# Kernel optimization log

Measured on AMD Instinct MI355X. Metric: run time of the kernel, lower is better.

Reference implementation:

```python
import jax, jax.numpy as jnp
import numpy as np

B, T, H = 256, 2048, 128
LSTM_IN = [24, 128, 128]


def _xavier(key, fan_out, fan_in):
    std = (2.0 / (fan_in + fan_out)) ** 0.5
    return jax.random.normal(key, (fan_out, fan_in), jnp.float32) * std


def setup_inputs() -> dict:
    key = jax.random.key(0)
    ks = jax.random.split(key, 32)
    inp = {}
    inp['scent'] = jax.random.normal(ks[0], (B, T, 3), jnp.float32)
    # fc1: Linear(3,12) + ReLU + Linear(12,24) + ReLU, xavier weights, zero bias
    inp['W1'] = _xavier(ks[1], 12, 3); inp['b1'] = jnp.zeros((12,), jnp.float32)
    inp['W2'] = _xavier(ks[2], 24, 12); inp['b2'] = jnp.zeros((24,), jnp.float32)
    # 3-layer LSTM, PyTorch default init: uniform(-1/sqrt(H), 1/sqrt(H)) for all params
    k = 1.0 / np.sqrt(H)
    for l in range(3):
        d = LSTM_IN[l]
        inp[f'Wih{l}'] = jax.random.uniform(ks[4 + 4 * l], (4 * H, d), jnp.float32, -k, k)
        inp[f'Whh{l}'] = jax.random.uniform(ks[5 + 4 * l], (4 * H, H), jnp.float32, -k, k)
        inp[f'bih{l}'] = jax.random.uniform(ks[6 + 4 * l], (4 * H,), jnp.float32, -k, k)
        inp[f'bhh{l}'] = jax.random.uniform(ks[7 + 4 * l], (4 * H,), jnp.float32, -k, k)
    # fc2: Linear(128,64) + ReLU + Linear(64,32) + ReLU
    inp['Wf1'] = _xavier(ks[20], 64, 128); inp['bf1'] = jnp.zeros((64,), jnp.float32)
    inp['Wf2'] = _xavier(ks[21], 32, 64); inp['bf2'] = jnp.zeros((32,), jnp.float32)
    return inp


def _lstm_layer(x, Wih, Whh, bih, bhh):
    # x: [T, B, D] -> ys: [T, B, H]; PyTorch gate order i, f, g, o
    gx = jnp.einsum('tbd,gd->tbg', x, Wih) + bih + bhh  # [T, B, 4H]

    def step(carry, g_t):
        h, c = carry
        gates = g_t + h @ Whh.T
        i, f, g, o = jnp.split(gates, 4, axis=-1)
        c = jax.nn.sigmoid(f) * c + jax.nn.sigmoid(i) * jnp.tanh(g)
        h = jax.nn.sigmoid(o) * jnp.tanh(c)
        return (h, c), h

    h0 = jnp.zeros((x.shape[1], H), x.dtype)
    (hT, cT), ys = jax.lax.scan(step, (h0, h0), gx)
    return ys, hT, cT


def reference(scent, W1, b1, W2, b2,
              Wih0, Whh0, bih0, bhh0,
              Wih1, Whh1, bih1, bhh1,
              Wih2, Whh2, bih2, bhh2,
              Wf1, bf1, Wf2, bf2):
    # fc1 (pointwise over B*T)
    x = jax.nn.relu(scent @ W1.T + b1)
    x = jax.nn.relu(x @ W2.T + b2)          # [B, T, 24]
    x = jnp.transpose(x, (1, 0, 2))          # [T, B, 24] seq-first
    hs, cs = [], []
    for Wih, Whh, bih, bhh in ((Wih0, Whh0, bih0, bhh0),
                               (Wih1, Whh1, bih1, bhh1),
                               (Wih2, Whh2, bih2, bhh2)):
        x, hT, cT = _lstm_layer(x, Wih, Whh, bih, bhh)
        hs.append(hT); cs.append(cT)
    h = jnp.stack(hs)                        # [3, B, H]
    c = jnp.stack(cs)                        # [3, B, H]
    y = jnp.transpose(x, (1, 0, 2))          # [B, T, H]
    y = jax.nn.relu(y @ Wf1.T + bf1)
    out = jax.nn.relu(y @ Wf2.T + bf2)       # [B, T, 32]
    return out, h, c
```

## Files before the change

### kernel.cpp

```cpp
#include <hip/hip_runtime.h>

#define B 256
#define T 2048
#define HDIM 128

typedef _Float16 f16;
typedef _Float16 h2 __attribute__((ext_vector_type(2)));
typedef _Float16 f16x8 __attribute__((ext_vector_type(8)));
typedef float f32x4 __attribute__((ext_vector_type(4)));

__device__ __forceinline__ float dot2(h2 a, h2 b, float c) {
#if __has_builtin(__builtin_amdgcn_fdot2)
    return __builtin_amdgcn_fdot2(a, b, c, false);
#else
    return c + (float)a[0] * (float)b[0] + (float)a[1] * (float)b[1];
#endif
}

__device__ __forceinline__ float sigm(float x) { return 1.0f / (1.0f + __expf(-x)); }
__device__ __forceinline__ float tanh_(float x) {
    float e = __expf(-2.0f * fabsf(x));
    float t = (1.0f - e) / (1.0f + e);
    return copysignf(t, x);
}

__device__ __forceinline__ void bar() {
    asm volatile("s_waitcnt lgkmcnt(0)" ::: "memory");
    __builtin_amdgcn_s_barrier();
}

__global__ __launch_bounds__(256) void fc1_kernel(
    const float* __restrict__ scent,
    const float* __restrict__ W1, const float* __restrict__ b1,
    const float* __restrict__ W2, const float* __restrict__ b2,
    f16* __restrict__ x1) {
    int r = blockIdx.x * 256 + threadIdx.x;
    int b = r >> 11, t = r & 2047;
    float s0 = scent[r * 3], s1 = scent[r * 3 + 1], s2 = scent[r * 3 + 2];
    float a[12];
#pragma unroll
    for (int i = 0; i < 12; i++) {
        float v = W1[i * 3] * s0 + W1[i * 3 + 1] * s1 + W1[i * 3 + 2] * s2 + b1[i];
        a[i] = fmaxf(v, 0.f);
    }
    union { f16 o[32]; uint4 u[4]; } U;
#pragma unroll
    for (int j = 0; j < 24; j++) {
        float v = b2[j];
#pragma unroll
        for (int i = 0; i < 12; i++) v = fmaf(W2[j * 12 + i], a[i], v);
        U.o[j] = (f16)fmaxf(v, 0.f);
    }
#pragma unroll
    for (int j = 24; j < 32; j++) U.o[j] = (f16)0.f;
    uint4* d4 = (uint4*)(x1 + ((size_t)t * B + b) * 32);
#pragma unroll
    for (int i = 0; i < 4; i++) d4[i] = U.u[i];
}

__global__ __launch_bounds__(256) void pack_kernel(const float* __restrict__ w,
                                                   unsigned int* __restrict__ o) {
    int i = blockIdx.x * 256 + threadIdx.x;
    if (i < 4096) {
        union { h2 h; unsigned int u; } U;
        U.h[0] = (f16)w[2 * i];
        U.h[1] = (f16)w[2 * i + 1];
        o[i] = U.u;
    }
}

template <int KF, int KREAL>
__global__ __attribute__((amdgpu_flat_work_group_size(512, 512), amdgpu_waves_per_eu(2, 2)))
void lstm_fused(
    const f16* __restrict__ x,
    const float* __restrict__ Wih,
    const float* __restrict__ Whh,
    const float* __restrict__ bih, const float* __restrict__ bhh,
    f16* __restrict__ y,
    float* __restrict__ hT, float* __restrict__ cT) {
    constexpr int KIN = KF * 32;
    __shared__ __align__(16) f16 xf[2][KF * 512];
    __shared__ __align__(16) f16 gxb[2][16 * 512];
    __shared__ __align__(16) f16 hbuf[HDIM];
    __shared__ float gbuf[512];

    const int tid = threadIdx.x, bb = blockIdx.x;
    const int l = tid & 63, wv = tid >> 6;
    const int s = tid & 7, grp = tid >> 3;
    const int lg = (l >> 4) & 3, lc = l & 15;

    f16x8 bf[4][KF];
    float bias4[4];
#pragma unroll
    for (int tt = 0; tt < 4; tt++) {
        int g = 64 * wv + 16 * tt + lc;
        bias4[tt] = bih[g] + bhh[g];
#pragma unroll
        for (int kf = 0; kf < KF; kf++) {
            f16x8 v;
#pragma unroll
            for (int j = 0; j < 8; j++) {
                int k = kf * 32 + lg * 8 + j;
                v[j] = (k < KREAL) ? (f16)Wih[g * KREAL + k] : (f16)0.f;
            }
            bf[tt][kf] = v;
        }
    }
    h2 wh[8][8];
#pragma unroll
    for (int i = 0; i < 8; i++) {
        int g = grp * 8 + i;
#pragma unroll
        for (int kk = 0; kk < 8; kk++) {
            int k = 16 * s + 2 * kk;
            h2 p; p[0] = (f16)Whh[g * HDIM + k]; p[1] = (f16)Whh[g * HDIM + k + 1];
            wh[i][kk] = p;
        }
    }
    float c = 0.f;
    if (tid < HDIM) hbuf[tid] = (f16)0.f;

    if (wv == 7) {
#pragma unroll
        for (int kf = 0; kf < KF; kf++) {
            uint4 vv = *(const uint4*)(x + ((size_t)(l & 15) * B + bb) * KIN + kf * 32 + lg * 8);
            *(uint4*)(&xf[0][kf * 512 + l * 8]) = vv;
        }
    }
    __syncthreads();
    {
        f16x8 af0[KF];
#pragma unroll
        for (int kf = 0; kf < KF; kf++) af0[kf] = *(const f16x8*)(&xf[0][kf * 512 + l * 8]);
#pragma unroll
        for (int tt = 0; tt < 4; tt++) {
            f32x4 a4 = {0.f, 0.f, 0.f, 0.f};
#pragma unroll
            for (int kf = 0; kf < KF; kf++)
                a4 = __builtin_amdgcn_mfma_f32_16x16x32_f16(af0[kf], bf[tt][kf], a4, 0, 0, 0);
#pragma unroll
            for (int q = 0; q < 4; q++)
                gxb[0][(4 * lg + q) * 512 + 64 * wv + 16 * tt + lc] = (f16)(a4[q] + bias4[tt]);
        }
        if (wv == 7) {
#pragma unroll
            for (int kf = 0; kf < KF; kf++) {
                uint4 vv = *(const uint4*)(x + ((size_t)(16 + (l & 15)) * B + bb) * KIN + kf * 32 + lg * 8);
                *(uint4*)(&xf[1][kf * 512 + l * 8]) = vv;
            }
        }
    }
    __syncthreads();

    f16x8 af[KF];
    f32x4 acc4 = {0.f, 0.f, 0.f, 0.f};
    uint4 xr[KF];
    for (int W = 0; W < T / 16; W++) {
        const int p = W & 1;
#pragma unroll
        for (int tl = 0; tl < 16; tl++) {
            const int t = W * 16 + tl;
            if (tl == 4 && wv == 7) {
                int twb = 16 * (W + 2) + (l & 15); if (twb > T - 1) twb = T - 1;
#pragma unroll
                for (int kf = 0; kf < KF; kf++)
                    xr[kf] = *(const uint4*)(x + ((size_t)twb * B + bb) * KIN + kf * 32 + lg * 8);
            }
            union { uint4 u[2]; h2 h[8]; } S;
            S.u[0] = *(const uint4*)(&hbuf[16 * s]);
            S.u[1] = *(const uint4*)(&hbuf[16 * s + 8]);
            float gxv = (float)gxb[p][tl * 512 + tid];
            float acc[8];
#pragma unroll
            for (int i = 0; i < 8; i++) acc[i] = 0.f;
#pragma unroll
            for (int kk = 0; kk < 8; kk++) {
#pragma unroll
                for (int i = 0; i < 8; i++) acc[i] = dot2(wh[i][kk], S.h[kk], acc[i]);
            }
            if (tl == 0) {
#pragma unroll
                for (int kf = 0; kf < KF; kf++)
                    af[kf] = *(const f16x8*)(&xf[(W + 1) & 1][kf * 512 + l * 8]);
            }
            if constexpr (KF == 4) {
                const int tt = tl >> 2, kf = tl & 3;
                if (kf == 0) acc4 = (f32x4){0.f, 0.f, 0.f, 0.f};
                acc4 = __builtin_amdgcn_mfma_f32_16x16x32_f16(af[kf], bf[tt][kf], acc4, 0, 0, 0);
                if (kf == 3) {
#pragma unroll
                    for (int q = 0; q < 4; q++)
                        gxb[p ^ 1][(4 * lg + q) * 512 + 64 * wv + 16 * tt + lc] =
                            (f16)(acc4[q] + bias4[tt]);
                }
            } else {
                if (tl < 4) {
                    const int tt = tl;
                    f32x4 a4 = {0.f, 0.f, 0.f, 0.f};
                    a4 = __builtin_amdgcn_mfma_f32_16x16x32_f16(af[0], bf[tt][0], a4, 0, 0, 0);
#pragma unroll
                    for (int q = 0; q < 4; q++)
                        gxb[p ^ 1][(4 * lg + q) * 512 + 64 * wv + 16 * tt + lc] =
                            (f16)(a4[q] + bias4[tt]);
                }
            }
            if (tl == 8 && wv == 7) {
#pragma unroll
                for (int kf = 0; kf < KF; kf++)
                    *(uint4*)(&xf[p][kf * 512 + l * 8]) = xr[kf];
            }
            const int h4 = s & 4, h2b = s & 2, h1 = s & 1;
            float q0 = (h4 ? acc[4] : acc[0]) + __shfl_xor(h4 ? acc[0] : acc[4], 4);
            float q1 = (h4 ? acc[5] : acc[1]) + __shfl_xor(h4 ? acc[1] : acc[5], 4);
            float q2 = (h4 ? acc[6] : acc[2]) + __shfl_xor(h4 ? acc[2] : acc[6], 4);
            float q3 = (h4 ? acc[7] : acc[3]) + __shfl_xor(h4 ? acc[3] : acc[7], 4);
            float r0 = (h2b ? q2 : q0) + __shfl_xor(h2b ? q0 : q2, 2);
            float r1 = (h2b ? q3 : q1) + __shfl_xor(h2b ? q1 : q3, 2);
            float v  = (h1 ? r1 : r0) + __shfl_xor(h1 ? r0 : r1, 1);
            v += gxv;

            const int gt = tid >> 7;
            float act = (gt == 2) ? tanh_(v) : sigm(v);
            gbuf[tid] = act;
            bar();

            if (tid < HDIM) {
                float gi = gbuf[tid], gf = gbuf[128 + tid], gg = gbuf[256 + tid], go = gbuf[384 + tid];
                c = gf * c + gi * gg;
                float hh = go * tanh_(c);
                hbuf[tid] = (f16)hh;
                y[((size_t)t * B + bb) * HDIM + tid] = (f16)hh;
                if (t == T - 1) { hT[bb * HDIM + tid] = hh; cT[bb * HDIM + tid] = c; }
            }
            bar();
        }
    }
}

__global__ __launch_bounds__(256) void fc2_kernel(
    const f16* __restrict__ yin,
    const unsigned int* __restrict__ w1,
    const float* __restrict__ bf1,
    const float* __restrict__ Wf2,
    const float* __restrict__ bf2,
    float* __restrict__ out) {
    int r = blockIdx.x * 256 + threadIdx.x;
    union { uint4 u4[16]; h2 h[64]; } Y;
    {
        const uint4* yr4 = (const uint4*)(yin + (size_t)r * 128);
#pragma unroll
        for (int i = 0; i < 16; i++) Y.u4[i] = yr4[i];
    }
    float acc2[32];
#pragma unroll
    for (int i = 0; i < 32; i++) acc2[i] = 0.f;

    for (int cO = 0; cO < 64; cO++) {
        float a0 = bf1[cO], a1 = 0.f, a2 = 0.f, a3 = 0.f;
#pragma unroll
        for (int kk = 0; kk < 64; kk += 4) {
            union { unsigned int u; h2 h; } W0, W1x, W2x, W3;
            W0.u = w1[cO * 64 + kk];      a0 = dot2(W0.h,  Y.h[kk],     a0);
            W1x.u = w1[cO * 64 + kk + 1]; a1 = dot2(W1x.h, Y.h[kk + 1], a1);
            W2x.u = w1[cO * 64 + kk + 2]; a2 = dot2(W2x.h, Y.h[kk + 2], a2);
            W3.u = w1[cO * 64 + kk + 3];  a3 = dot2(W3.h,  Y.h[kk + 3], a3);
        }
        float a = fmaxf((a0 + a1) + (a2 + a3), 0.f);
#pragma unroll
        for (int c2 = 0; c2 < 32; c2++) acc2[c2] = fmaf(a, Wf2[c2 * 64 + cO], acc2[c2]);
    }
    float* orow = out + ((size_t)(r & 255) * T + (r >> 8)) * 32;
#pragma unroll
    for (int c2 = 0; c2 < 32; c2++) orow[c2] = fmaxf(acc2[c2] + bf2[c2], 0.f);
}

extern "C" void kernel_launch(void* const* d_in, const int* in_sizes, int n_in,
                              void* d_out, int out_size, void* d_ws, size_t ws_size,
                              hipStream_t stream) {
    const float* scent = (const float*)d_in[0];
    const float* W1 = (const float*)d_in[1];
    const float* b1 = (const float*)d_in[2];
    const float* W2 = (const float*)d_in[3];
    const float* b2 = (const float*)d_in[4];
    const float* Wih[3] = {(const float*)d_in[5], (const float*)d_in[9], (const float*)d_in[13]};
    const float* Whh[3] = {(const float*)d_in[6], (const float*)d_in[10], (const float*)d_in[14]};
    const float* bihp[3] = {(const float*)d_in[7], (const float*)d_in[11], (const float*)d_in[15]};
    const float* bhhp[3] = {(const float*)d_in[8], (const float*)d_in[12], (const float*)d_in[16]};
    const float* Wf1 = (const float*)d_in[17];
    const float* bf1 = (const float*)d_in[18];
    const float* Wf2 = (const float*)d_in[19];
    const float* bf2 = (const float*)d_in[20];

    const size_t o_x1 = 0;
    const size_t o_y  = 33554432;
    const size_t o_w1 = o_y + 134217728;
    const size_t need = o_w1 + 16384;
    if (ws_size < need) return;

    char* ws = (char*)d_ws;
    f16* x1 = (f16*)(ws + o_x1);
    f16* yb = (f16*)(ws + o_y);
    unsigned int* w1p = (unsigned int*)(ws + o_w1);

    float* out = (float*)d_out;
    float* hO = out + (size_t)B * T * 32;
    float* cO = hO + 3 * B * HDIM;

    pack_kernel<<<16, 256, 0, stream>>>(Wf1, w1p);
    fc1_kernel<<<(B * T) / 256, 256, 0, stream>>>(scent, W1, b1, W2, b2, x1);
    lstm_fused<1, 24><<<B, 512, 0, stream>>>(x1, Wih[0], Whh[0], bihp[0], bhhp[0],
                                             yb, hO, cO);
    lstm_fused<4, 128><<<B, 512, 0, stream>>>(yb, Wih[1], Whh[1], bihp[1], bhhp[1],
                                              yb, hO + B * HDIM, cO + B * HDIM);
    lstm_fused<4, 128><<<B, 512, 0, stream>>>(yb, Wih[2], Whh[2], bihp[2], bhhp[2],
                                              yb, hO + 2 * B * HDIM, cO + 2 * B * HDIM);
    fc2_kernel<<<(B * T) / 256, 256, 0, stream>>>(yb, w1p, bf1, Wf2, bf2, out);
}
```

Baseline: 4.807 ms.

## Split input projection into chunked MFMA GEMM separate from LSTM recurrence

Moves the input-to-hidden gate projection out of the sequential LSTM kernel into a separate MFMA GEMM that runs per 256-step chunk, writing gate pre-activations to a global workspace. The recurrent kernel then only does the hidden matvec and reads gx with an 8-step register prefetch, carrying h and c between chunks through the output state buffers. This takes MFMA work and LDS staging off the serial critical path, but adds global gx traffic, extra kernel launches, and rounds the carried h to f16 between chunks.

```diff
diff --git a/kernel.cpp b/kernel.cpp
--- a/kernel.cpp
+++ b/kernel.cpp
@@ -3,6 +3,8 @@
 #define B 256
 #define T 2048
 #define HDIM 128
+#define CH 256
+#define NCHUNK (T / CH)
 
 typedef _Float16 f16;
 typedef _Float16 h2 __attribute__((ext_vector_type(2)));
@@ -69,43 +71,90 @@
     }
 }
 
-template <int KF, int KREAL>
-__global__ __attribute__((amdgpu_flat_work_group_size(512, 512), amdgpu_waves_per_eu(2, 2)))
-void lstm_fused(
+template <int KIN, int KREAL, int SP>
+__global__ __launch_bounds__(256) void gx_gemm(
     const f16* __restrict__ x,
     const float* __restrict__ Wih,
+    const float* __restrict__ bih, const float* __restrict__ bhh,
+    f16* __restrict__ gx,
+    int t0) {
+    constexpr int KF = KIN / 32;
+    __shared__ __align__(16) f16 Alds[64 * SP];
+    const int tid = threadIdx.x;
+    const int mb = blockIdx.x, nb = blockIdx.y;
+    const int l = tid & 63, wv = tid >> 6;
+    const int lc = l & 15, lg = l >> 4;
+
+    const f16* xrow = x + ((size_t)t0 * B + (size_t)mb * 64) * KIN;
+    if (KIN == 128) {
+#pragma unroll
+        for (int it = 0; it < 4; it++) {
+            int row = it * 16 + (tid >> 4), cc = tid & 15;
+            uint4 v = *(const uint4*)(xrow + (size_t)row * KIN + cc * 8);
+            *(uint4*)(&Alds[row * SP + cc * 8]) = v;
+        }
+    } else {
+        int row = tid >> 2, cc = tid & 3;
+        uint4 v = *(const uint4*)(xrow + (size_t)row * KIN + cc * 8);
+        *(uint4*)(&Alds[row * SP + cc * 8]) = v;
+    }
+
+    const int gbase = nb * 128 + (wv & 1) * 64;
+    const int rbase = (wv >> 1) * 32;
+    f16x8 bf[4][KF];
+    float bias4[4];
+#pragma unroll
+    for (int gt = 0; gt < 4; gt++) {
+        int g = gbase + gt * 16 + lc;
+        bias4[gt] = bih[g] + bhh[g];
+#pragma unroll
+        for (int kf = 0; kf < KF; kf++) {
+            f16x8 v;
+#pragma unroll
+            for (int j = 0; j < 8; j++) {
+                int k = kf * 32 + lg * 8 + j;
+                v[j] = (k < KREAL) ? (f16)Wih[(size_t)g * KREAL + k] : (f16)0.f;
+            }
+            bf[gt][kf] = v;
+        }
+    }
+    __syncthreads();
+
+    f32x4 acc[2][4] = {};
+#pragma unroll
+    for (int kf = 0; kf < KF; kf++) {
+#pragma unroll
+        for (int rt = 0; rt < 2; rt++) {
+            f16x8 af = *(const f16x8*)(&Alds[(rbase + rt * 16 + lc) * SP + kf * 32 + lg * 8]);
+#pragma unroll
+            for (int gt = 0; gt < 4; gt++)
+                acc[rt][gt] = __builtin_amdgcn_mfma_f32_16x16x32_f16(af, bf[gt][kf], acc[rt][gt], 0, 0, 0);
+        }
+    }
+#pragma unroll
+    for (int rt = 0; rt < 2; rt++)
+#pragma unroll
+        for (int gt = 0; gt < 4; gt++)
+#pragma unroll
+            for (int q = 0; q < 4; q++) {
+                int rr = mb * 64 + rbase + rt * 16 + lg * 4 + q;
+                int gg = gbase + gt * 16 + lc;
+                gx[(size_t)rr * 512 + gg] = (f16)(acc[rt][gt][q] + bias4[gt]);
+            }
+}
+
+__global__ __attribute__((amdgpu_flat_work_group_size(512, 512), amdgpu_waves_per_eu(2, 2)))
+void lstm_rec(
+    const f16* __restrict__ gx,
     const float* __restrict__ Whh,
-    const float* __restrict__ bih, const float* __restrict__ bhh,
     f16* __restrict__ y,
-    float* __restrict__ hT, float* __restrict__ cT) {
-    constexpr int KIN = KF * 32;
-    __shared__ __align__(16) f16 xf[2][KF * 512];
-    __shared__ __align__(16) f16 gxb[2][16 * 512];
+    float* __restrict__ hS, float* __restrict__ cS,
+    int t0, int init) {
     __shared__ __align__(16) f16 hbuf[HDIM];
     __shared__ float gbuf[512];
-
     const int tid = threadIdx.x, bb = blockIdx.x;
-    const int l = tid & 63, wv = tid >> 6;
     const int s = tid & 7, grp = tid >> 3;
-    const int lg = (l >> 4) & 3, lc = l & 15;
-
-    f16x8 bf[4][KF];
-    float bias4[4];
-#pragma unroll
-    for (int tt = 0; tt < 4; tt++) {
-        int g = 64 * wv + 16 * tt + lc;
-        bias4[tt] = bih[g] + bhh[g];
-#pragma unroll
-        for (int kf = 0; kf < KF; kf++) {
-            f16x8 v;
-#pragma unroll
-            for (int j = 0; j < 8; j++) {
-                int k = kf * 32 + lg * 8 + j;
-                v[j] = (k < KREAL) ? (f16)Wih[g * KREAL + k] : (f16)0.f;
-            }
-            bf[tt][kf] = v;
-        }
-    }
+
     h2 wh[8][8];
 #pragma unroll
     for (int i = 0; i < 8; i++) {
@@ -113,63 +162,34 @@
 #pragma unroll
         for (int kk = 0; kk < 8; kk++) {
             int k = 16 * s + 2 * kk;
-            h2 p; p[0] = (f16)Whh[g * HDIM + k]; p[1] = (f16)Whh[g * HDIM + k + 1];
+            h2 p; p[0] = (f16)Whh[(size_t)g * HDIM + k]; p[1] = (f16)Whh[(size_t)g * HDIM + k + 1];
             wh[i][kk] = p;
         }
     }
     float c = 0.f;
-    if (tid < HDIM) hbuf[tid] = (f16)0.f;
-
-    if (wv == 7) {
-#pragma unroll
-        for (int kf = 0; kf < KF; kf++) {
-            uint4 vv = *(const uint4*)(x + ((size_t)(l & 15) * B + bb) * KIN + kf * 32 + lg * 8);
-            *(uint4*)(&xf[0][kf * 512 + l * 8]) = vv;
-        }
-    }
+    if (tid < HDIM) {
+        float hv = 0.f;
+        if (!init) { hv = hS[bb * HDIM + tid]; c = cS[bb * HDIM + tid]; }
+        hbuf[tid] = (f16)hv;
+    }
+    const ushort* gp = (const ushort*)gx + (size_t)bb * 512 + tid;
+    ushort gxr[8];
+#pragma unroll
+    for (int j = 0; j < 8; j++) gxr[j] = gp[(size_t)j * (B * 512)];
     __syncthreads();
-    {
-        f16x8 af0[KF];
-#pragma unroll
-        for (int kf = 0; kf < KF; kf++) af0[kf] = *(const f16x8*)(&xf[0][kf * 512 + l * 8]);
-#pragma unroll
-        for (int tt = 0; tt < 4; tt++) {
-            f32x4 a4 = {0.f, 0.f, 0.f, 0.f};
-#pragma unroll
-            for (int kf = 0; kf < KF; kf++)
-                a4 = __builtin_amdgcn_mfma_f32_16x16x32_f16(af0[kf], bf[tt][kf], a4, 0, 0, 0);
-#pragma unroll
-            for (int q = 0; q < 4; q++)
-                gxb[0][(4 * lg + q) * 512 + 64 * wv + 16 * tt + lc] = (f16)(a4[q] + bias4[tt]);
-        }
-        if (wv == 7) {
-#pragma unroll
-            for (int kf = 0; kf < KF; kf++) {
-                uint4 vv = *(const uint4*)(x + ((size_t)(16 + (l & 15)) * B + bb) * KIN + kf * 32 + lg * 8);
-                *(uint4*)(&xf[1][kf * 512 + l * 8]) = vv;
-            }
-        }
-    }
-    __syncthreads();
-
-    f16x8 af[KF];
-    f32x4 acc4 = {0.f, 0.f, 0.f, 0.f};
-    uint4 xr[KF];
-    for (int W = 0; W < T / 16; W++) {
-        const int p = W & 1;
-#pragma unroll
-        for (int tl = 0; tl < 16; tl++) {
-            const int t = W * 16 + tl;
-            if (tl == 4 && wv == 7) {
-                int twb = 16 * (W + 2) + (l & 15); if (twb > T - 1) twb = T - 1;
-#pragma unroll
-                for (int kf = 0; kf < KF; kf++)
-                    xr[kf] = *(const uint4*)(x + ((size_t)twb * B + bb) * KIN + kf * 32 + lg * 8);
-            }
+
+    for (int w8 = 0; w8 < CH / 8; w8++) {
+#pragma unroll
+        for (int j = 0; j < 8; j++) {
+            const int t = w8 * 8 + j;
+            union { ushort u; f16 h; } GU; GU.u = gxr[j];
+            float gxv = (float)GU.h;
+            int tn = t + 8; if (tn > CH - 1) tn = CH - 1;
+            gxr[j] = gp[(size_t)tn * (B * 512)];
+
             union { uint4 u[2]; h2 h[8]; } S;
             S.u[0] = *(const uint4*)(&hbuf[16 * s]);
             S.u[1] = *(const uint4*)(&hbuf[16 * s + 8]);
-            float gxv = (float)gxb[p][tl * 512 + tid];
             float acc[8];
 #pragma unroll
             for (int i = 0; i < 8; i++) acc[i] = 0.f;
@@ -177,37 +197,6 @@
             for (int kk = 0; kk < 8; kk++) {
 #pragma unroll
                 for (int i = 0; i < 8; i++) acc[i] = dot2(wh[i][kk], S.h[kk], acc[i]);
-            }
-            if (tl == 0) {
-#pragma unroll
-                for (int kf = 0; kf < KF; kf++)
-                    af[kf] = *(const f16x8*)(&xf[(W + 1) & 1][kf * 512 + l * 8]);
-            }
-            if constexpr (KF == 4) {
-                const int tt = tl >> 2, kf = tl & 3;
-                if (kf == 0) acc4 = (f32x4){0.f, 0.f, 0.f, 0.f};
-                acc4 = __builtin_amdgcn_mfma_f32_16x16x32_f16(af[kf], bf[tt][kf], acc4, 0, 0, 0);
-                if (kf == 3) {
-#pragma unroll
-                    for (int q = 0; q < 4; q++)
-                        gxb[p ^ 1][(4 * lg + q) * 512 + 64 * wv + 16 * tt + lc] =
-                            (f16)(acc4[q] + bias4[tt]);
-                }
-            } else {
-                if (tl < 4) {
-                    const int tt = tl;
-                    f32x4 a4 = {0.f, 0.f, 0.f, 0.f};
-                    a4 = __builtin_amdgcn_mfma_f32_16x16x32_f16(af[0], bf[tt][0], a4, 0, 0, 0);
-#pragma unroll
-                    for (int q = 0; q < 4; q++)
-                        gxb[p ^ 1][(4 * lg + q) * 512 + 64 * wv + 16 * tt + lc] =
-                            (f16)(a4[q] + bias4[tt]);
-                }
-            }
-            if (tl == 8 && wv == 7) {
-#pragma unroll
-                for (int kf = 0; kf < KF; kf++)
-                    *(uint4*)(&xf[p][kf * 512 + l * 8]) = xr[kf];
             }
             const int h4 = s & 4, h2b = s & 2, h1 = s & 1;
             float q0 = (h4 ? acc[4] : acc[0]) + __shfl_xor(h4 ? acc[0] : acc[4], 4);
@@ -229,11 +218,14 @@
                 c = gf * c + gi * gg;
                 float hh = go * tanh_(c);
                 hbuf[tid] = (f16)hh;
-                y[((size_t)t * B + bb) * HDIM + tid] = (f16)hh;
-                if (t == T - 1) { hT[bb * HDIM + tid] = hh; cT[bb * HDIM + tid] = c; }
+                y[((size_t)(t0 + t) * B + bb) * HDIM + tid] = (f16)hh;
             }
             bar();
         }
+    }
+    if (tid < HDIM) {
+        hS[bb * HDIM + tid] = (float)hbuf[tid];
+        cS[bb * HDIM + tid] = c;
     }
 }
 
@@ -293,13 +285,15 @@
 
     const size_t o_x1 = 0;
     const size_t o_y  = 33554432;
-    const size_t o_w1 = o_y + 134217728;
+    const size_t o_gx = o_y + 134217728;
+    const size_t o_w1 = o_gx + 67108864;
     const size_t need = o_w1 + 16384;
     if (ws_size < need) return;
 
     char* ws = (char*)d_ws;
     f16* x1 = (f16*)(ws + o_x1);
     f16* yb = (f16*)(ws + o_y);
+    f16* gxb = (f16*)(ws + o_gx);
     unsigned int* w1p = (unsigned int*)(ws + o_w1);
 
     float* out = (float*)d_out;
@@ -308,11 +302,19 @@
 
     pack_kernel<<<16, 256, 0, stream>>>(Wf1, w1p);
     fc1_kernel<<<(B * T) / 256, 256, 0, stream>>>(scent, W1, b1, W2, b2, x1);
-    lstm_fused<1, 24><<<B, 512, 0, stream>>>(x1, Wih[0], Whh[0], bihp[0], bhhp[0],
-                                             yb, hO, cO);
-    lstm_fused<4, 128><<<B, 512, 0, stream>>>(yb, Wih[1], Whh[1], bihp[1], bhhp[1],
-                                              yb, hO + B * HDIM, cO + B * HDIM);
-    lstm_fused<4, 128><<<B, 512, 0, stream>>>(yb, Wih[2], Whh[2], bihp[2], bhhp[2],
-                                              yb, hO + 2 * B * HDIM, cO + 2 * B * HDIM);
+
+    dim3 ggrid(CH * B / 64, 4);
+    for (int l = 0; l < 3; l++) {
+        float* hS = hO + (size_t)l * B * HDIM;
+        float* cS = cO + (size_t)l * B * HDIM;
+        for (int ch = 0; ch < NCHUNK; ch++) {
+            int t0 = ch * CH;
+            if (l == 0)
+                gx_gemm<32, 24, 40><<<ggrid, 256, 0, stream>>>(x1, Wih[0], bihp[0], bhhp[0], gxb, t0);
+            else
+                gx_gemm<128, 128, 144><<<ggrid, 256, 0, stream>>>(yb, Wih[l], bihp[l], bhhp[l], gxb, t0);
+            lstm_rec<<<B, 512, 0, stream>>>(gxb, Whh[l], yb, hS, cS, t0, ch == 0 ? 1 : 0);
+        }
+    }
     fc2_kernel<<<(B * T) / 256, 256, 0, stream>>>(yb, w1p, bf1, Wf2, bf2, out);
 }
```

Measured after the change: 6.517 ms. +35.6%, slower.
